# Performance work log

Hardware: AMD Instinct MI355X
Metric: run time of the kernel (lower is better)

The kernel has to match this reference:

```python
import jax, jax.numpy as jnp
import numpy as np

N_NODES = 50000
N_EDGES = 800000
IN_CH = 128
EDGE_DIM = 16
N_GRAPHS = 500


def _lin_params(key, din, dout):
    k1, k2 = jax.random.split(key)
    s = 1.0 / np.sqrt(din)
    W = jax.random.uniform(k1, (din, dout), jnp.float32, -s, s)
    b = jax.random.uniform(k2, (dout,), jnp.float32, -s, s)
    return W, b


def setup_inputs() -> dict:
    key = jax.random.key(0)
    ks = jax.random.split(key, 20)
    x = jax.random.normal(ks[0], (N_NODES, IN_CH), jnp.float32)
    edge_attr = jax.random.normal(ks[1], (N_EDGES, EDGE_DIM), jnp.float32)
    edge_index = jax.random.randint(ks[2], (2, N_EDGES), 0, N_NODES, jnp.int32)
    n_nodes = jnp.full((N_GRAPHS,), N_NODES // N_GRAPHS, jnp.int32)
    inp = {"x": x, "edge_attr": edge_attr, "edge_index": edge_index, "n_nodes": n_nodes}
    # conv1: edge lin (edge_dim->128), mlp 128->256->256, bn 256
    inp["We1"], inp["be1"] = _lin_params(ks[3], EDGE_DIM, IN_CH)
    inp["W11"], inp["b11"] = _lin_params(ks[4], IN_CH, 256)
    inp["W12"], inp["b12"] = _lin_params(ks[5], 256, 256)
    inp["g1"], inp["bt1"] = jnp.ones((256,), jnp.float32), jnp.zeros((256,), jnp.float32)
    # conv2: edge lin (edge_dim->256), mlp 256->128->128, bn 128
    inp["We2"], inp["be2"] = _lin_params(ks[6], EDGE_DIM, 256)
    inp["W21"], inp["b21"] = _lin_params(ks[7], 256, 128)
    inp["W22"], inp["b22"] = _lin_params(ks[8], 128, 128)
    inp["g2"], inp["bt2"] = jnp.ones((128,), jnp.float32), jnp.zeros((128,), jnp.float32)
    # conv3: edge lin (edge_dim->128), mlp 128->64->64, bn 64
    inp["We3"], inp["be3"] = _lin_params(ks[9], EDGE_DIM, 128)
    inp["W31"], inp["b31"] = _lin_params(ks[10], 128, 64)
    inp["W32"], inp["b32"] = _lin_params(ks[11], 64, 64)
    inp["g3"], inp["bt3"] = jnp.ones((64,), jnp.float32), jnp.zeros((64,), jnp.float32)
    # head
    inp["Wf1"], inp["bf1"] = _lin_params(ks[12], 64, 16)
    inp["Wf2"], inp["bf2"] = _lin_params(ks[13], 16, 1)
    return inp


def _gine(x, src, dst, ea_proj, W1, b1, W2, b2):
    # message: relu(x_j + lin(edge_attr)); aggregate: scatter-add; GIN0 eps=0
    m = jax.nn.relu(x[src] + ea_proj)                      # [E, D]
    agg = jax.ops.segment_sum(m, dst, num_segments=N_NODES)
    h = x + agg
    return jax.nn.relu(h @ W1 + b1) @ W2 + b2


def _bn(x, g, b):
    mu = x.mean(axis=0)
    var = x.var(axis=0)
    return (x - mu) * jax.lax.rsqrt(var + 1e-5) * g + b


def reference(x, edge_attr, edge_index, n_nodes,
              We1, be1, W11, b11, W12, b12, g1, bt1,
              We2, be2, W21, b21, W22, b22, g2, bt2,
              We3, be3, W31, b31, W32, b32, g3, bt3,
              Wf1, bf1, Wf2, bf2):
    src, dst = edge_index[0], edge_index[1]
    h = _gine(x, src, dst, edge_attr @ We1 + be1, W11, b11, W12, b12)
    h = _bn(jax.nn.relu(h), g1, bt1)
    h = _gine(h, src, dst, edge_attr @ We2 + be2, W21, b21, W22, b22)
    h = _bn(jax.nn.relu(h), g2, bt2)
    h = _gine(h, src, dst, edge_attr @ We3 + be3, W31, b31, W32, b32)
    h = _bn(jax.nn.relu(h), g3, bt3)
    last_idx = jnp.cumsum(n_nodes) - 1                      # [G]
    master = h[last_idx]                                    # [G, 64]; dropout = identity (eval)
    out = jax.nn.relu(master @ Wf1 + bf1) @ Wf2 + bf2       # [G, 1]
    return out
```

## Files before the change

kernel.cpp:

```cpp
#include <hip/hip_runtime.h>
#include <hip/hip_bf16.h>


typedef __attribute__((ext_vector_type(8))) short short8;
typedef __attribute__((ext_vector_type(4))) float floatx4;
typedef __attribute__((ext_vector_type(2))) float float2v;

__device__ __forceinline__ float2v splat2(float s) {
    float2v v;
    v[0] = s;
    v[1] = s;
    return v;
}

__device__ __forceinline__ ushort f2bf_rne(float x) {
    unsigned u = __float_as_uint(x);
    unsigned r = (u + 0x7FFFu + ((u >> 16) & 1u)) >> 16;
    return (ushort)r;
}


__global__ __launch_bounds__(256) void hist_kernel(const int* __restrict__ dst,
                                                   int* __restrict__ deg, int E) {
    int i = blockIdx.x * blockDim.x + threadIdx.x;
    int stride = gridDim.x * blockDim.x;
    for (; i < E; i += stride) atomicAdd(&deg[dst[i]], 1);
}

__global__ __launch_bounds__(1024) void scan_kernel(const int* __restrict__ deg,
                                                    int* __restrict__ row_start, int N) {
    __shared__ int part[1024];
    int tid = threadIdx.x;
    int per = (N + 1023) / 1024;
    int start = tid * per;
    int end = min(start + per, N);
    int s = 0;
    for (int i = start; i < end; ++i) s += deg[i];
    part[tid] = s;
    __syncthreads();
    if (tid == 0) {
        int t = 0;
        for (int i = 0; i < 1024; ++i) {
            int v = part[i];
            part[i] = t;
            t += v;
        }
    }
    __syncthreads();
    int run = part[tid];
    for (int i = start; i < end; ++i) {
        row_start[i] = run;
        run += deg[i];
    }
    if (tid == 1023) row_start[N] = run;
}

__global__ __launch_bounds__(256) void scatter_kernel(
    const int* __restrict__ src, const int* __restrict__ dst,
    const int* __restrict__ row_start, int* __restrict__ cursor,
    int* __restrict__ csr_eid, int* __restrict__ csr_src, int E) {
    int i = blockIdx.x * blockDim.x + threadIdx.x;
    int stride = gridDim.x * blockDim.x;
    for (; i < E; i += stride) {
        int v = dst[i];
        int p = row_start[v] + atomicAdd(&cursor[v], 1);
        csr_eid[p] = i;
        csr_src[p] = src[i];
    }
}

__device__ __forceinline__ void wsplit(const float* W, ushort* Wth, ushort* Wtl,
                                       int K, int N, int t) {
    int k = t / N, n = t - k * N;
    float v = W[t];
    ushort hv = f2bf_rne(v);
    float hf = __uint_as_float(((unsigned)hv) << 16);
    ushort lv = f2bf_rne(v - hf);
    Wth[(size_t)n * K + k] = hv;
    Wtl[(size_t)n * K + k] = lv;
}

__global__ __launch_bounds__(256) void prep_all(
    const float* W11, ushort* W11h, ushort* W11l,
    const float* W12, ushort* W12h, ushort* W12l,
    const float* W21, ushort* W21h, ushort* W21l,
    const float* W22, ushort* W22h, ushort* W22l,
    const float* W31, ushort* W31h, ushort* W31l,
    const float* W32, ushort* W32h, ushort* W32l) {
    int t = blockIdx.x * blockDim.x + threadIdx.x;
    const int s1 = 128 * 256, s2 = s1 + 256 * 256, s3 = s2 + 256 * 128;
    const int s4 = s3 + 128 * 128, s5 = s4 + 128 * 64, s6 = s5 + 64 * 64;
    if (t < s1) wsplit(W11, W11h, W11l, 128, 256, t);
    else if (t < s2) wsplit(W12, W12h, W12l, 256, 256, t - s1);
    else if (t < s3) wsplit(W21, W21h, W21l, 256, 128, t - s2);
    else if (t < s4) wsplit(W22, W22h, W22l, 128, 128, t - s3);
    else if (t < s5) wsplit(W31, W31h, W31l, 128, 64, t - s4);
    else if (t < s6) wsplit(W32, W32h, W32l, 64, 64, t - s5);
}

template <int D>
__global__ __launch_bounds__(256)
__attribute__((amdgpu_waves_per_eu(4, 4))) void gine_agg_kernel(
    const float* __restrict__ h, const float* __restrict__ ea,
    const int* __restrict__ row_start, const int* __restrict__ csr_eid,
    const int* __restrict__ csr_src,
    const float* __restrict__ We, const float* __restrict__ be,
    ushort* __restrict__ uhi, ushort* __restrict__ ulo, int N) {
    constexpr int C2 = D / 128;
    const int lane = threadIdx.x & 63;

    float2v w[16][C2];
#pragma unroll
    for (int k = 0; k < 16; ++k)
#pragma unroll
        for (int c = 0; c < C2; ++c)
            w[k][c] = ((const float2v*)&We[k * D])[c * 64 + lane];
    float2v bias[C2];
#pragma unroll
    for (int c = 0; c < C2; ++c) bias[c] = ((const float2v*)be)[c * 64 + lane];

    int v = blockIdx.x * 4 + (threadIdx.x >> 6);
    const int vstride = gridDim.x * 4;
    const float2v z2 = splat2(0.f);

    for (; v < N; v += vstride) {
        int e0 = row_start[v];
        int e1 = row_start[v + 1];
        float2v acc[C2];
#pragma unroll
        for (int c = 0; c < C2; ++c) acc[c] = z2;

        int i = e0;
        for (; i + 4 <= e1; i += 4) {
            int myeid = csr_eid[i + (lane >> 4)];
            float eav = ea[(size_t)myeid * 16 + (lane & 15)];
            int s0 = csr_src[i + 0];
            int s1 = csr_src[i + 1];
            int s2 = csr_src[i + 2];
            int s3 = csr_src[i + 3];
            float2v hv[4][C2];
#pragma unroll
            for (int c = 0; c < C2; ++c) {
                int idx = c * 64 + lane;
                hv[0][c] = ((const float2v*)(h + (size_t)s0 * D))[idx];
                hv[1][c] = ((const float2v*)(h + (size_t)s1 * D))[idx];
                hv[2][c] = ((const float2v*)(h + (size_t)s2 * D))[idx];
                hv[3][c] = ((const float2v*)(h + (size_t)s3 * D))[idx];
            }
#pragma unroll
            for (int e = 0; e < 4; ++e) {
                float wk[16];
#pragma unroll
                for (int k = 0; k < 16; ++k)
                    wk[k] = __int_as_float(
                        __builtin_amdgcn_readlane(__float_as_int(eav), e * 16 + k));
#pragma unroll
                for (int c = 0; c < C2; ++c) {
                    float2v p = bias[c];
#pragma unroll
                    for (int k = 0; k < 16; ++k)
                        p = __builtin_elementwise_fma(splat2(wk[k]), w[k][c], p);
                    float2v m = p + hv[e][c];
                    acc[c] += __builtin_elementwise_max(m, z2);
                }
            }
        }
        for (; i < e1; ++i) {
            int eid = csr_eid[i];
            int s = csr_src[i];
            float eav = (lane < 16) ? ea[(size_t)eid * 16 + lane] : 0.f;
            float wk[16];
#pragma unroll
            for (int k = 0; k < 16; ++k)
                wk[k] = __int_as_float(
                    __builtin_amdgcn_readlane(__float_as_int(eav), k));
#pragma unroll
            for (int c = 0; c < C2; ++c) {
                float2v p = bias[c];
#pragma unroll
                for (int k = 0; k < 16; ++k)
                    p = __builtin_elementwise_fma(splat2(wk[k]), w[k][c], p);
                float2v m = p + ((const float2v*)(h + (size_t)s * D))[c * 64 + lane];
                acc[c] += __builtin_elementwise_max(m, z2);
            }
        }
#pragma unroll
        for (int c = 0; c < C2; ++c) {
            float2v uv = ((const float2v*)(h + (size_t)v * D))[c * 64 + lane] + acc[c];
            ushort h0 = f2bf_rne(uv[0]);
            ushort h1 = f2bf_rne(uv[1]);
            float hf0 = __uint_as_float(((unsigned)h0) << 16);
            float hf1 = __uint_as_float(((unsigned)h1) << 16);
            ushort l0 = f2bf_rne(uv[0] - hf0);
            ushort l1 = f2bf_rne(uv[1] - hf1);
            size_t o = (size_t)v * D + c * 128 + lane * 2;
            *(ushort2*)&uhi[o] = make_ushort2(h0, h1);
            *(ushort2*)&ulo[o] = make_ushort2(l0, l1);
        }
    }
}

template <int WRITE_BF16, int STATS>
__global__ __launch_bounds__(256) void gemm_mfma(
    const ushort* __restrict__ Ah, const ushort* __restrict__ Al,
    const ushort* __restrict__ Bh, const ushort* __restrict__ Bl,
    const float* __restrict__ bias,
    float* __restrict__ Cf, ushort* __restrict__ Chi, ushort* __restrict__ Clo,
    float* __restrict__ stats, int Nreal,
    int N, int K, int relu) {
    __shared__ ushort sA[2][128][72];
    __shared__ ushort sB[2][64][72];
    const int tid = threadIdx.x;
    const int wave = tid >> 6, lane = tid & 63;
    const int lrow = lane & 15, lquad = lane >> 4;
    const int bm = blockIdx.y * 128;
    const int bn = blockIdx.x * 64;

    floatx4 acc[2][4];
#pragma unroll
    for (int i = 0; i < 2; ++i)
#pragma unroll
        for (int j = 0; j < 4; ++j) acc[i][j] = (floatx4)0.f;

    for (int k0 = 0; k0 < K; k0 += 64) {
        for (int s = tid; s < 1024; s += 256) {
            int row = s >> 3, c8 = (s & 7) * 8;
            size_t g = (size_t)(bm + row) * K + k0 + c8;
            *(int4*)&sA[0][row][c8] = *(const int4*)&Ah[g];
            *(int4*)&sA[1][row][c8] = *(const int4*)&Al[g];
        }
        for (int s = tid; s < 512; s += 256) {
            int row = s >> 3, c8 = (s & 7) * 8;
            size_t g = (size_t)(bn + row) * K + k0 + c8;
            *(int4*)&sB[0][row][c8] = *(const int4*)&Bh[g];
            *(int4*)&sB[1][row][c8] = *(const int4*)&Bl[g];
        }
        __syncthreads();
        const int rb = wave * 32;
#pragma unroll
        for (int kk = 0; kk < 2; ++kk) {
            int ko = kk * 32 + lquad * 8;
            short8 ah[2], al[2], bh[4], bl[4];
#pragma unroll
            for (int i = 0; i < 2; ++i) {
                ah[i] = *(const short8*)&sA[0][rb + i * 16 + lrow][ko];
                al[i] = *(const short8*)&sA[1][rb + i * 16 + lrow][ko];
            }
#pragma unroll
            for (int j = 0; j < 4; ++j) {
                bh[j] = *(const short8*)&sB[0][j * 16 + lrow][ko];
                bl[j] = *(const short8*)&sB[1][j * 16 + lrow][ko];
            }
#pragma unroll
            for (int i = 0; i < 2; ++i)
#pragma unroll
                for (int j = 0; j < 4; ++j) {
                    acc[i][j] = __builtin_amdgcn_mfma_f32_16x16x32_bf16(
                        ah[i], bh[j], acc[i][j], 0, 0, 0);
                    acc[i][j] = __builtin_amdgcn_mfma_f32_16x16x32_bf16(
                        ah[i], bl[j], acc[i][j], 0, 0, 0);
                    acc[i][j] = __builtin_amdgcn_mfma_f32_16x16x32_bf16(
                        al[i], bh[j], acc[i][j], 0, 0, 0);
                }
        }
        __syncthreads();
    }
    float sj[4] = {0.f, 0.f, 0.f, 0.f};
    float qj[4] = {0.f, 0.f, 0.f, 0.f};
#pragma unroll
    for (int i = 0; i < 2; ++i)
#pragma unroll
        for (int j = 0; j < 4; ++j) {
            int gc = bn + j * 16 + lrow;
            float bv = bias[gc];
#pragma unroll
            for (int r = 0; r < 4; ++r) {
                int gr = bm + wave * 32 + i * 16 + lquad * 4 + r;
                float v = acc[i][j][r] + bv;
                if (relu) v = fmaxf(v, 0.f);
                if (STATS && gr < Nreal) {
                    sj[j] += v;
                    qj[j] = fmaf(v, v, qj[j]);
                }
                if (WRITE_BF16) {
                    ushort hv = f2bf_rne(v);
                    float hf = __uint_as_float(((unsigned)hv) << 16);
                    ushort lv = f2bf_rne(v - hf);
                    Chi[(size_t)gr * N + gc] = hv;
                    Clo[(size_t)gr * N + gc] = lv;
                } else {
                    Cf[(size_t)gr * N + gc] = v;
                }
            }
        }
    if (STATS) {
#pragma unroll
        for (int j = 0; j < 4; ++j) {
            float s = sj[j], q = qj[j];
            s += __shfl_xor(s, 16);
            s += __shfl_xor(s, 32);
            q += __shfl_xor(q, 16);
            q += __shfl_xor(q, 32);
            if (lquad == 0) {
                int gc = bn + j * 16 + lrow;
                atomicAdd(&stats[gc], s);
                atomicAdd(&stats[N + gc], q);
            }
        }
    }
}

__global__ __launch_bounds__(256) void bn_apply_kernel(
    const float* __restrict__ r, float* __restrict__ h,
    const float* __restrict__ sums,
    const float* __restrict__ g, const float* __restrict__ bt,
    int N, int D, int Dm1) {
    int idx = blockIdx.x * blockDim.x + threadIdx.x;
    int total = N * D;
    int stride = gridDim.x * blockDim.x;
    float invN = 1.0f / (float)N;
    for (; idx < total; idx += stride) {
        int c = idx & Dm1;
        float mu = sums[c] * invN;
        float var = fmaf(-mu, mu, sums[D + c] * invN);
        float sc = rsqrtf(var + 1e-5f) * g[c];
        h[idx] = (r[idx] - mu) * sc + bt[c];
    }
}

__global__ void head_kernel(const float* __restrict__ h, const int* __restrict__ n_nodes,
                            const float* __restrict__ Wf1, const float* __restrict__ bf1,
                            const float* __restrict__ Wf2, const float* __restrict__ bf2,
                            float* __restrict__ out, int G) {
    int g = blockIdx.x * blockDim.x + threadIdx.x;
    if (g >= G) return;
    int s = 0;
    for (int i = 0; i <= g; ++i) s += n_nodes[i];
    const float* m = &h[(size_t)(s - 1) * 64];
    float o = bf2[0];
#pragma unroll 4
    for (int j = 0; j < 16; ++j) {
        float acc = bf1[j];
        for (int k = 0; k < 64; ++k) acc = fmaf(m[k], Wf1[k * 16 + j], acc);
        acc = fmaxf(acc, 0.f);
        o = fmaf(acc, Wf2[j], o);
    }
    out[g] = o;
}

extern "C" void kernel_launch(void* const* d_in, const int* in_sizes, int n_in,
                              void* d_out, int out_size, void* d_ws, size_t ws_size,
                              hipStream_t stream) {
    const float* x = (const float*)d_in[0];
    const float* ea = (const float*)d_in[1];
    const int* eidx = (const int*)d_in[2];
    const int* n_nodes = (const int*)d_in[3];
    const float* We1 = (const float*)d_in[4];
    const float* be1 = (const float*)d_in[5];
    const float* W11 = (const float*)d_in[6];
    const float* b11 = (const float*)d_in[7];
    const float* W12 = (const float*)d_in[8];
    const float* b12 = (const float*)d_in[9];
    const float* g1 = (const float*)d_in[10];
    const float* bt1 = (const float*)d_in[11];
    const float* We2 = (const float*)d_in[12];
    const float* be2 = (const float*)d_in[13];
    const float* W21 = (const float*)d_in[14];
    const float* b21 = (const float*)d_in[15];
    const float* W22 = (const float*)d_in[16];
    const float* b22 = (const float*)d_in[17];
    const float* g2 = (const float*)d_in[18];
    const float* bt2 = (const float*)d_in[19];
    const float* We3 = (const float*)d_in[20];
    const float* be3 = (const float*)d_in[21];
    const float* W31 = (const float*)d_in[22];
    const float* b31 = (const float*)d_in[23];
    const float* W32 = (const float*)d_in[24];
    const float* b32 = (const float*)d_in[25];
    const float* g3 = (const float*)d_in[26];
    const float* bt3 = (const float*)d_in[27];
    const float* Wf1 = (const float*)d_in[28];
    const float* bf1 = (const float*)d_in[29];
    const float* Wf2 = (const float*)d_in[30];
    const float* bf2 = (const float*)d_in[31];

    const int N = in_sizes[0] / 128;
    const int E = in_sizes[2] / 2;
    const int G = in_sizes[3];
    const int Mp = ((N + 127) / 128) * 128;
    const int* srcp = eidx;
    const int* dstp = eidx + E;

    float* H = (float*)d_ws;
    float* UR = H + (size_t)Mp * 256;
    float* TT = UR + (size_t)Mp * 256;
    float* stats1 = TT + (size_t)Mp * 256;
    float* stats2 = stats1 + 512;
    float* stats3 = stats2 + 256;
    int* deg = (int*)(stats3 + 128);
    int* cursor = deg + N;
    int* row_start = cursor + N;
    int* csr_eid = row_start + N + 1;
    int* csr_src = csr_eid + E;
    size_t woff = (size_t)(csr_src + E - (int*)d_ws);
    woff = (woff + 3) & ~(size_t)3;
    ushort* wp = (ushort*)((int*)d_ws + woff);
    ushort* W11th = wp; wp += 128 * 256;
    ushort* W11tl = wp; wp += 128 * 256;
    ushort* W12th = wp; wp += 256 * 256;
    ushort* W12tl = wp; wp += 256 * 256;
    ushort* W21th = wp; wp += 256 * 128;
    ushort* W21tl = wp; wp += 256 * 128;
    ushort* W22th = wp; wp += 128 * 128;
    ushort* W22tl = wp; wp += 128 * 128;
    ushort* W31th = wp; wp += 128 * 64;
    ushort* W31tl = wp; wp += 128 * 64;
    ushort* W32th = wp; wp += 64 * 64;
    ushort* W32tl = wp; wp += 64 * 64;

    hipMemsetAsync(stats1, 0, 896 * sizeof(float) + (size_t)2 * N * sizeof(int), stream);

    const int prepTot = 128 * 256 + 256 * 256 + 256 * 128 + 128 * 128 + 128 * 64 + 64 * 64;
    prep_all<<<(prepTot + 255) / 256, 256, 0, stream>>>(
        W11, W11th, W11tl, W12, W12th, W12tl, W21, W21th, W21tl,
        W22, W22th, W22tl, W31, W31th, W31tl, W32, W32th, W32tl);

    hist_kernel<<<3125, 256, 0, stream>>>(dstp, deg, E);
    scan_kernel<<<1, 1024, 0, stream>>>(deg, row_start, N);
    scatter_kernel<<<3125, 256, 0, stream>>>(srcp, dstp, row_start, cursor,
                                             csr_eid, csr_src, E);

    const int aggBlocks = (N + 3) / 4;
    const int gy = Mp / 128;
    float* R = UR;

    {
        ushort* Uhi = (ushort*)UR; ushort* Ulo = Uhi + (size_t)Mp * 128;
        ushort* Thi = (ushort*)TT; ushort* Tlo = Thi + (size_t)Mp * 256;
        gine_agg_kernel<128><<<aggBlocks, 256, 0, stream>>>(
            x, ea, row_start, csr_eid, csr_src, We1, be1, Uhi, Ulo, N);
        gemm_mfma<1, 0><<<dim3(4, gy), 256, 0, stream>>>(
            Uhi, Ulo, W11th, W11tl, b11, nullptr, Thi, Tlo, nullptr, 0, 256, 128, 1);
        gemm_mfma<0, 1><<<dim3(4, gy), 256, 0, stream>>>(
            Thi, Tlo, W12th, W12tl, b12, R, nullptr, nullptr, stats1, N, 256, 256, 1);
        bn_apply_kernel<<<2048, 256, 0, stream>>>(R, H, stats1, g1, bt1, N, 256, 255);
    }

    {
        ushort* Uhi = (ushort*)UR; ushort* Ulo = Uhi + (size_t)Mp * 256;
        ushort* Thi = (ushort*)TT; ushort* Tlo = Thi + (size_t)Mp * 128;
        gine_agg_kernel<256><<<aggBlocks, 256, 0, stream>>>(
            H, ea, row_start, csr_eid, csr_src, We2, be2, Uhi, Ulo, N);
        gemm_mfma<1, 0><<<dim3(2, gy), 256, 0, stream>>>(
            Uhi, Ulo, W21th, W21tl, b21, nullptr, Thi, Tlo, nullptr, 0, 128, 256, 1);
        gemm_mfma<0, 1><<<dim3(2, gy), 256, 0, stream>>>(
            Thi, Tlo, W22th, W22tl, b22, R, nullptr, nullptr, stats2, N, 128, 128, 1);
        bn_apply_kernel<<<2048, 256, 0, stream>>>(R, H, stats2, g2, bt2, N, 128, 127);
    }

    {
        ushort* Uhi = (ushort*)UR; ushort* Ulo = Uhi + (size_t)Mp * 128;
        ushort* Thi = (ushort*)TT; ushort* Tlo = Thi + (size_t)Mp * 64;
        gine_agg_kernel<128><<<aggBlocks, 256, 0, stream>>>(
            H, ea, row_start, csr_eid, csr_src, We3, be3, Uhi, Ulo, N);
        gemm_mfma<1, 0><<<dim3(1, gy), 256, 0, stream>>>(
            Uhi, Ulo, W31th, W31tl, b31, nullptr, Thi, Tlo, nullptr, 0, 64, 128, 1);
        gemm_mfma<0, 1><<<dim3(1, gy), 256, 0, stream>>>(
            Thi, Tlo, W32th, W32tl, b32, R, nullptr, nullptr, stats3, N, 64, 64, 1);
        bn_apply_kernel<<<2048, 256, 0, stream>>>(R, H, stats3, g3, bt3, N, 64, 63);
    }

    head_kernel<<<(G + 255) / 256, 256, 0, stream>>>(H, n_nodes, Wf1, bf1, Wf2, bf2,
                                                     (float*)d_out, G);
}
```

Before: 1.055 ms.

## Gather neighbor features from a bf16 copy in GINE aggregation

Keeps a bf16 copy of the node features, produced by a new conversion kernel for the input and by the BN-apply kernel for later layers. The edge aggregation kernel reads neighbors from this copy, which roughly halves the bytes of the dominant random-gather traffic. Lanes are remapped to own contiguous channel groups so each can load them with one vector access, and the forced waves-per-EU attribute is dropped. In exchange there are extra conversion writes, and neighbor messages lose precision against the fp32 reference. The bf16 buffer aliases the GEMM temporary buffer.

Result: faster. 1.009 ms (-4.4%).

```diff
diff --git a/kernel.cpp b/kernel.cpp
--- a/kernel.cpp
+++ b/kernel.cpp
@@ -7,16 +7,17 @@
 typedef __attribute__((ext_vector_type(2))) float float2v;
 
 __device__ __forceinline__ float2v splat2(float s) {
-    float2v v;
-    v[0] = s;
-    v[1] = s;
-    return v;
+    float2v v; v[0] = s; v[1] = s; return v;
 }
 
 __device__ __forceinline__ ushort f2bf_rne(float x) {
     unsigned u = __float_as_uint(x);
     unsigned r = (u + 0x7FFFu + ((u >> 16) & 1u)) >> 16;
     return (ushort)r;
+}
+
+__device__ __forceinline__ float bf2f(ushort u) {
+    return __uint_as_float(((unsigned)u) << 16);
 }
 
 
@@ -74,7 +75,7 @@
     int k = t / N, n = t - k * N;
     float v = W[t];
     ushort hv = f2bf_rne(v);
-    float hf = __uint_as_float(((unsigned)hv) << 16);
+    float hf = bf2f(hv);
     ushort lv = f2bf_rne(v - hf);
     Wth[(size_t)n * K + k] = hv;
     Wtl[(size_t)n * K + k] = lv;
@@ -98,26 +99,43 @@
     else if (t < s6) wsplit(W32, W32h, W32l, 64, 64, t - s5);
 }
 
+__global__ __launch_bounds__(256) void f32_to_bf16(const float* __restrict__ in,
+                                                   ushort* __restrict__ out, long n4) {
+    long i = (long)blockIdx.x * blockDim.x + threadIdx.x;
+    long stride = (long)gridDim.x * blockDim.x;
+    for (; i < n4; i += stride) {
+        float4 v = ((const float4*)in)[i];
+        ushort4 o;
+        o.x = f2bf_rne(v.x);
+        o.y = f2bf_rne(v.y);
+        o.z = f2bf_rne(v.z);
+        o.w = f2bf_rne(v.w);
+        ((ushort4*)out)[i] = o;
+    }
+}
+
 template <int D>
-__global__ __launch_bounds__(256)
-__attribute__((amdgpu_waves_per_eu(4, 4))) void gine_agg_kernel(
-    const float* __restrict__ h, const float* __restrict__ ea,
+__global__ __launch_bounds__(256) void gine_agg_kernel(
+    const float* __restrict__ h, const ushort* __restrict__ hb,
+    const float* __restrict__ ea,
     const int* __restrict__ row_start, const int* __restrict__ csr_eid,
     const int* __restrict__ csr_src,
     const float* __restrict__ We, const float* __restrict__ be,
     ushort* __restrict__ uhi, ushort* __restrict__ ulo, int N) {
-    constexpr int C2 = D / 128;
+    constexpr int CPL = D / 64;
+    constexpr int C2 = CPL / 2;
     const int lane = threadIdx.x & 63;
+    const int ch0 = lane * CPL;
 
     float2v w[16][C2];
 #pragma unroll
     for (int k = 0; k < 16; ++k)
 #pragma unroll
         for (int c = 0; c < C2; ++c)
-            w[k][c] = ((const float2v*)&We[k * D])[c * 64 + lane];
+            w[k][c] = *(const float2v*)&We[k * D + ch0 + 2 * c];
     float2v bias[C2];
 #pragma unroll
-    for (int c = 0; c < C2; ++c) bias[c] = ((const float2v*)be)[c * 64 + lane];
+    for (int c = 0; c < C2; ++c) bias[c] = *(const float2v*)&be[ch0 + 2 * c];
 
     int v = blockIdx.x * 4 + (threadIdx.x >> 6);
     const int vstride = gridDim.x * 4;
@@ -134,18 +152,25 @@
         for (; i + 4 <= e1; i += 4) {
             int myeid = csr_eid[i + (lane >> 4)];
             float eav = ea[(size_t)myeid * 16 + (lane & 15)];
-            int s0 = csr_src[i + 0];
-            int s1 = csr_src[i + 1];
-            int s2 = csr_src[i + 2];
-            int s3 = csr_src[i + 3];
+            int se[4];
+            se[0] = csr_src[i + 0];
+            se[1] = csr_src[i + 1];
+            se[2] = csr_src[i + 2];
+            se[3] = csr_src[i + 3];
             float2v hv[4][C2];
 #pragma unroll
-            for (int c = 0; c < C2; ++c) {
-                int idx = c * 64 + lane;
-                hv[0][c] = ((const float2v*)(h + (size_t)s0 * D))[idx];
-                hv[1][c] = ((const float2v*)(h + (size_t)s1 * D))[idx];
-                hv[2][c] = ((const float2v*)(h + (size_t)s2 * D))[idx];
-                hv[3][c] = ((const float2v*)(h + (size_t)s3 * D))[idx];
+            for (int e = 0; e < 4; ++e) {
+                if (CPL == 4) {
+                    ushort4 r = *(const ushort4*)&hb[(size_t)se[e] * D + ch0];
+                    hv[e][0][0] = bf2f(r.x);
+                    hv[e][0][1] = bf2f(r.y);
+                    hv[e][C2 - 1][0] = bf2f(r.z);
+                    hv[e][C2 - 1][1] = bf2f(r.w);
+                } else {
+                    ushort2 r = *(const ushort2*)&hb[(size_t)se[e] * D + ch0];
+                    hv[e][0][0] = bf2f(r.x);
+                    hv[e][0][1] = bf2f(r.y);
+                }
             }
 #pragma unroll
             for (int e = 0; e < 4; ++e) {
@@ -174,28 +199,49 @@
             for (int k = 0; k < 16; ++k)
                 wk[k] = __int_as_float(
                     __builtin_amdgcn_readlane(__float_as_int(eav), k));
+            float2v hv[C2];
+            if (CPL == 4) {
+                ushort4 r = *(const ushort4*)&hb[(size_t)s * D + ch0];
+                hv[0][0] = bf2f(r.x);
+                hv[0][1] = bf2f(r.y);
+                hv[C2 - 1][0] = bf2f(r.z);
+                hv[C2 - 1][1] = bf2f(r.w);
+            } else {
+                ushort2 r = *(const ushort2*)&hb[(size_t)s * D + ch0];
+                hv[0][0] = bf2f(r.x);
+                hv[0][1] = bf2f(r.y);
+            }
 #pragma unroll
             for (int c = 0; c < C2; ++c) {
                 float2v p = bias[c];
 #pragma unroll
                 for (int k = 0; k < 16; ++k)
                     p = __builtin_elementwise_fma(splat2(wk[k]), w[k][c], p);
-                float2v m = p + ((const float2v*)(h + (size_t)s * D))[c * 64 + lane];
+                float2v m = p + hv[c];
                 acc[c] += __builtin_elementwise_max(m, z2);
             }
         }
+        ushort hi[CPL], lo[CPL];
 #pragma unroll
         for (int c = 0; c < C2; ++c) {
-            float2v uv = ((const float2v*)(h + (size_t)v * D))[c * 64 + lane] + acc[c];
-            ushort h0 = f2bf_rne(uv[0]);
-            ushort h1 = f2bf_rne(uv[1]);
-            float hf0 = __uint_as_float(((unsigned)h0) << 16);
-            float hf1 = __uint_as_float(((unsigned)h1) << 16);
-            ushort l0 = f2bf_rne(uv[0] - hf0);
-            ushort l1 = f2bf_rne(uv[1] - hf1);
-            size_t o = (size_t)v * D + c * 128 + lane * 2;
-            *(ushort2*)&uhi[o] = make_ushort2(h0, h1);
-            *(ushort2*)&ulo[o] = make_ushort2(l0, l1);
+            float2v sv = *(const float2v*)&h[(size_t)v * D + ch0 + 2 * c];
+#pragma unroll
+            for (int j = 0; j < 2; ++j) {
+                float uv = sv[j] + acc[c][j];
+                ushort hu = f2bf_rne(uv);
+                ushort lu = f2bf_rne(uv - bf2f(hu));
+                hi[2 * c + j] = hu;
+                lo[2 * c + j] = lu;
+            }
+        }
+        if (CPL == 4) {
+            *(ushort4*)&uhi[(size_t)v * D + ch0] =
+                make_ushort4(hi[0], hi[1], hi[CPL - 2], hi[CPL - 1]);
+            *(ushort4*)&ulo[(size_t)v * D + ch0] =
+                make_ushort4(lo[0], lo[1], lo[CPL - 2], lo[CPL - 1]);
+        } else {
+            *(ushort2*)&uhi[(size_t)v * D + ch0] = make_ushort2(hi[0], hi[1]);
+            *(ushort2*)&ulo[(size_t)v * D + ch0] = make_ushort2(lo[0], lo[1]);
         }
     }
 }
@@ -284,8 +330,7 @@
                 }
                 if (WRITE_BF16) {
                     ushort hv = f2bf_rne(v);
-                    float hf = __uint_as_float(((unsigned)hv) << 16);
-                    ushort lv = f2bf_rne(v - hf);
+                    ushort lv = f2bf_rne(v - bf2f(hv));
                     Chi[(size_t)gr * N + gc] = hv;
                     Clo[(size_t)gr * N + gc] = lv;
                 } else {
@@ -312,6 +357,7 @@
 
 __global__ __launch_bounds__(256) void bn_apply_kernel(
     const float* __restrict__ r, float* __restrict__ h,
+    ushort* __restrict__ hbout,
     const float* __restrict__ sums,
     const float* __restrict__ g, const float* __restrict__ bt,
     int N, int D, int Dm1) {
@@ -324,7 +370,9 @@
         float mu = sums[c] * invN;
         float var = fmaf(-mu, mu, sums[D + c] * invN);
         float sc = rsqrtf(var + 1e-5f) * g[c];
-        h[idx] = (r[idx] - mu) * sc + bt[c];
+        float val = (r[idx] - mu) * sc + bt[c];
+        h[idx] = val;
+        if (hbout) hbout[idx] = f2bf_rne(val);
     }
 }
 
@@ -433,41 +481,43 @@
     const int aggBlocks = (N + 3) / 4;
     const int gy = Mp / 128;
     float* R = UR;
+    ushort* HB = (ushort*)TT;
 
     {
         ushort* Uhi = (ushort*)UR; ushort* Ulo = Uhi + (size_t)Mp * 128;
         ushort* Thi = (ushort*)TT; ushort* Tlo = Thi + (size_t)Mp * 256;
+        f32_to_bf16<<<2048, 256, 0, stream>>>(x, HB, (long)N * 128 / 4);
         gine_agg_kernel<128><<<aggBlocks, 256, 0, stream>>>(
-            x, ea, row_start, csr_eid, csr_src, We1, be1, Uhi, Ulo, N);
+            x, HB, ea, row_start, csr_eid, csr_src, We1, be1, Uhi, Ulo, N);
         gemm_mfma<1, 0><<<dim3(4, gy), 256, 0, stream>>>(
             Uhi, Ulo, W11th, W11tl, b11, nullptr, Thi, Tlo, nullptr, 0, 256, 128, 1);
         gemm_mfma<0, 1><<<dim3(4, gy), 256, 0, stream>>>(
             Thi, Tlo, W12th, W12tl, b12, R, nullptr, nullptr, stats1, N, 256, 256, 1);
-        bn_apply_kernel<<<2048, 256, 0, stream>>>(R, H, stats1, g1, bt1, N, 256, 255);
+        bn_apply_kernel<<<2048, 256, 0, stream>>>(R, H, HB, stats1, g1, bt1, N, 256, 255);
     }
 
     {
         ushort* Uhi = (ushort*)UR; ushort* Ulo = Uhi + (size_t)Mp * 256;
         ushort* Thi = (ushort*)TT; ushort* Tlo = Thi + (size_t)Mp * 128;
         gine_agg_kernel<256><<<aggBlocks, 256, 0, stream>>>(
-            H, ea, row_start, csr_eid, csr_src, We2, be2, Uhi, Ulo, N);
+            H, HB, ea, row_start, csr_eid, csr_src, We2, be2, Uhi, Ulo, N);
         gemm_mfma<1, 0><<<dim3(2, gy), 256, 0, stream>>>(
             Uhi, Ulo, W21th, W21tl, b21, nullptr, Thi, Tlo, nullptr, 0, 128, 256, 1);
         gemm_mfma<0, 1><<<dim3(2, gy), 256, 0, stream>>>(
             Thi, Tlo, W22th, W22tl, b22, R, nullptr, nullptr, stats2, N, 128, 128, 1);
-        bn_apply_kernel<<<2048, 256, 0, stream>>>(R, H, stats2, g2, bt2, N, 128, 127);
+        bn_apply_kernel<<<2048, 256, 0, stream>>>(R, H, HB, stats2, g2, bt2, N, 128, 127);
     }
 
     {
         ushort* Uhi = (ushort*)UR; ushort* Ulo = Uhi + (size_t)Mp * 128;
         ushort* Thi = (ushort*)TT; ushort* Tlo = Thi + (size_t)Mp * 64;
         gine_agg_kernel<128><<<aggBlocks, 256, 0, stream>>>(
-            H, ea, row_start, csr_eid, csr_src, We3, be3, Uhi, Ulo, N);
+            H, HB, ea, row_start, csr_eid, csr_src, We3, be3, Uhi, Ulo, N);
         gemm_mfma<1, 0><<<dim3(1, gy), 256, 0, stream>>>(
             Uhi, Ulo, W31th, W31tl, b31, nullptr, Thi, Tlo, nullptr, 0, 64, 128, 1);
         gemm_mfma<0, 1><<<dim3(1, gy), 256, 0, stream>>>(
             Thi, Tlo, W32th, W32tl, b32, R, nullptr, nullptr, stats3, N, 64, 64, 1);
-        bn_apply_kernel<<<2048, 256, 0, stream>>>(R, H, stats3, g3, bt3, N, 64, 63);
+        bn_apply_kernel<<<2048, 256, 0, stream>>>(R, H, nullptr, stats3, g3, bt3, N, 64, 63);
     }
 
     head_kernel<<<(G + 255) / 256, 256, 0, stream>>>(H, n_nodes, Wf1, bf1, Wf2, bf2,
```
